# Kernel tuning notes

Measured on AMD Instinct MI355X. Metric: run time of the kernel, lower is better.

## Reference

```python
import jax, jax.numpy as jnp
import numpy as np

N, E, H, ED = 10000, 160000, 512, 16
EPS = 1e-5
EDGE_SCALE = 0.1

def _ln(x, g, b):
    mu = jnp.mean(x, axis=-1, keepdims=True)
    var = jnp.mean(jnp.square(x - mu), axis=-1, keepdims=True)
    return (x - mu) * jax.lax.rsqrt(var + EPS) * g + b

def setup_inputs() -> dict:
    key = jax.random.key(0)
    ks = jax.random.split(key, 16)
    def w(k, i, o):
        return jax.random.normal(k, (i, o), jnp.float32) * (1.0 / np.sqrt(i))
    return {
        "h": jax.random.normal(ks[0], (N, H), jnp.float32),
        "edge_attr": jax.random.normal(ks[1], (E, ED), jnp.float32),
        "msg_w1": w(ks[2], H + ED, H), "msg_b1": jnp.zeros((H,), jnp.float32),
        "msg_w2": w(ks[3], H, H),      "msg_b2": jnp.zeros((H,), jnp.float32),
        "upd_w1": w(ks[4], 2 * H, H),  "upd_b1": jnp.zeros((H,), jnp.float32),
        "upd_w2": w(ks[5], H, H),      "upd_b2": jnp.zeros((H,), jnp.float32),
        "norm_g": jnp.ones((H,), jnp.float32), "norm_b": jnp.zeros((H,), jnp.float32),
        "em_w1": w(ks[6], 2 * H + ED, ED), "em_b1": jnp.zeros((ED,), jnp.float32),
        "em_w2": w(ks[7], ED, ED),         "em_b2": jnp.zeros((ED,), jnp.float32),
        "eg_w": w(ks[8], 2 * H + ED, 1),   "eg_b": jnp.zeros((1,), jnp.float32),
        "en_g": jnp.ones((ED,), jnp.float32), "en_b": jnp.zeros((ED,), jnp.float32),
        "edge_index": jax.random.randint(ks[9], (2, E), 0, N, jnp.int32),
    }

def reference(h, edge_attr, msg_w1, msg_b1, msg_w2, msg_b2,
              upd_w1, upd_b1, upd_w2, upd_b2, norm_g, norm_b,
              em_w1, em_b1, em_w2, em_b2, eg_w, eg_b, en_g, en_b,
              edge_index):
    src, dst = edge_index[0], edge_index[1]
    hs = h[src]                      # (E, H)
    hd = h[dst]                      # (E, H)
    # edge update with gating + scaled residual (eval: keep mask == 1)
    z = jnp.concatenate([hs, hd, edge_attr], axis=-1)   # (E, 2H+ED)
    gate = jax.nn.sigmoid(z @ eg_w + eg_b)               # (E, 1)
    delta = jax.nn.gelu(z @ em_w1 + em_b1, approximate=False) @ em_w2 + em_b2
    e_new = _ln(edge_attr + EDGE_SCALE * gate * delta, en_g, en_b)
    # message computation + scatter-add aggregation
    zm = jnp.concatenate([hs, e_new], axis=-1)           # (E, H+ED)
    m = jax.nn.gelu(zm @ msg_w1 + msg_b1, approximate=False) @ msg_w2 + msg_b2
    agg = jax.ops.segment_sum(m, dst, num_segments=h.shape[0])  # (N, H)
    # node update + residual + LayerNorm
    zu = jnp.concatenate([h, agg], axis=-1)              # (N, 2H)
    h2 = jax.nn.gelu(zu @ upd_w1 + upd_b1, approximate=False) @ upd_w2 + upd_b2
    h_out = _ln(h + h2, norm_g, norm_b)
    return (h_out, e_new)
```

## Files before the change

kernel.cpp:

```cpp
#include <hip/hip_runtime.h>

#define N_NODES 10000
#define N_EDGES 160000
#define HD 512
#define EDD 16

typedef unsigned short u16;
typedef __attribute__((ext_vector_type(8))) short bf16x8;
typedef __attribute__((ext_vector_type(4))) float f32x4;
typedef unsigned int u32;

__device__ __forceinline__ float bf2f(u16 u){
  unsigned int x = ((unsigned int)u) << 16;
  return __builtin_bit_cast(float, x);
}
__device__ __forceinline__ u16 f2bf(float f){
  unsigned int x = __builtin_bit_cast(unsigned int, f);
  unsigned int r = (x + 0x7fffu + ((x >> 16) & 1u)) >> 16;
  return (u16)r;
}
__device__ __forceinline__ float ldx(const void* p, long long i, int f32){
  return f32 ? ((const float*)p)[i] : bf2f(((const u16*)p)[i]);
}
__device__ __forceinline__ void stx(void* p, long long i, int f32, float v){
  if (f32) ((float*)p)[i] = v; else ((u16*)p)[i] = f2bf(v);
}
__device__ __forceinline__ float gelu_f(float x){
  float c = x * x;
  float a = x * (1.5957691216f + 0.0713548162f * c);
  float e = __expf(-a);
  return x * __builtin_amdgcn_rcpf(1.0f + e);
}
__device__ __forceinline__ f32x4 mfma16(bf16x8 a, bf16x8 b, f32x4 c){
  return __builtin_amdgcn_mfma_f32_16x16x32_bf16(a, b, c, 0, 0, 0);
}
__device__ __forceinline__ int swz8(int row, int slot){
  return (slot ^ ((row >> 1) & 3)) * 8;
}
__device__ __forceinline__ bf16x8 ld8(const void* p, long long i, int f32){
  if (!f32) return *(const bf16x8*)((const u16*)p + i);
  const float* q = (const float*)p + i;
  float4 a = *(const float4*)q, b = *(const float4*)(q + 4);
  u16 t[8] = { f2bf(a.x), f2bf(a.y), f2bf(a.z), f2bf(a.w),
               f2bf(b.x), f2bf(b.y), f2bf(b.z), f2bf(b.w) };
  return *(const bf16x8*)t;
}
__device__ __forceinline__ void stage8(const void* src, long long idx, int f32, u16* dst){
  bf16x8 v = ld8(src, idx, f32);
  *(bf16x8*)dst = v;
}

__device__ __forceinline__ int probe_rand(const void* p, int l){
  const u16* q = (const u16*)p;
  float mx = 0.f;
  #pragma unroll
  for (int i = 0; i < 4; ++i) mx = fmaxf(mx, fabsf(bf2f(q[l * 4 + i])));
  #pragma unroll
  for (int m = 1; m < 64; m <<= 1) mx = fmaxf(mx, __shfl_xor(mx, m, 64));
  return (mx > 1e3f) ? 1 : 0;
}
__global__ __launch_bounds__(64) void kprobe(
    const void* h, const void* ea, const void* mw1, const void* mw2,
    const void* uw1, const void* uw2, const void* ew1, const void* ew2,
    const void* egw, const void* ng, const void* eng, int* F)
{
  const int l = threadIdx.x;
  int f0 = probe_rand(h, l),   f1 = probe_rand(ea, l),  f2 = probe_rand(mw1, l);
  int f3 = probe_rand(mw2, l), f4 = probe_rand(uw1, l), f5 = probe_rand(uw2, l);
  int f6 = probe_rand(ew1, l), f7 = probe_rand(ew2, l), f8 = probe_rand(egw, l);
  if (l == 0){
    F[0] = f0; F[1] = f1; F[2] = f2; F[3] = f3; F[4] = f4; F[5] = f5;
    F[6] = f6; F[7] = f7; F[8] = f8;
    F[9]  = (((const u16*)ng)[0]  == 0) ? 1 : 0;
    F[10] = (((const u16*)eng)[0] == 0) ? 1 : 0;
    F[11] = f0;
  }
}

__global__ void kfill(u16* __restrict__ out, long long n, float val){
  long long i = (long long)blockIdx.x * 256 + threadIdx.x;
  if (i < n) out[i] = f2bf(val);
}

__global__ __launch_bounds__(256) void kprep(
    const void* __restrict__ h, const void* __restrict__ mw1,
    const void* __restrict__ ew1, const void* __restrict__ egw,
    const void* __restrict__ mb2, const void* __restrict__ uw1,
    const int* __restrict__ F,
    u16* __restrict__ hB, u16* __restrict__ W1T, u16* __restrict__ WceT,
    float* __restrict__ bfused)
{
  __shared__ float tl[64][65];
  const int b = blockIdx.x, tid = threadIdx.x;
  if (b < 2500){
    const long long i = ((long long)b * 256 + tid) * 8;
    if (i < (long long)N_NODES * HD)
      *(bf16x8*)(hB + i) = ld8(h, i, F[0]);
  } else if (b < 2572){
    const int b2 = b - 2500;
    const int kt0 = (b2 >> 3) * 64, nt0 = (b2 & 7) * 64;
    const int ty = tid >> 6, tx = tid & 63;
    const int fw = F[2];
    #pragma unroll
    for (int q = 0; q < 16; ++q){
      const int r = ty * 16 + q;
      const int sr = kt0 + r;
      tl[r][tx] = (sr < 528) ? ldx(mw1, (long long)sr * 512 + nt0 + tx, fw) : 0.f;
    }
    __syncthreads();
    #pragma unroll
    for (int q = 0; q < 16; ++q){
      const int r = ty * 16 + q;
      const int k = kt0 + tx;
      if (k < 544) W1T[(size_t)(nt0 + r) * 544 + k] = f2bf(tl[tx][r]);
    }
  } else if (b < 2668){
    const int i = (b - 2572) * 256 + tid;
    const int c = i >> 9, k = i & 511;
    float v = 0.f;
    if (c < 16)       v = ldx(ew1, (long long)k * 16 + c, F[6]);
    else if (c < 32)  v = ldx(ew1, (long long)(512 + k) * 16 + (c - 16), F[6]);
    else if (c == 32) v = ldx(egw, k, F[8]);
    else if (c == 33) v = ldx(egw, 512 + k, F[8]);
    WceT[i] = f2bf(v);
  } else {
    float* ls   = &tl[0][0];
    float* part = &tl[0][0] + 1024;
    const int f3 = F[3], f4 = F[4];
    for (int j = tid; j < 512; j += 256) ls[j] = ldx(mb2, j, f3);
    __syncthreads();
    const int nn = tid & 31, jg = tid >> 5;
    const int n = (b - 2668) * 32 + nn;
    float a = 0.f;
    for (int jj = 0; jj < 64; ++jj){
      const int j = jg * 64 + jj;
      a += ls[j] * ldx(uw1, (long long)(512 + j) * 512 + n, f4);
    }
    part[jg * 33 + nn] = a;
    __syncthreads();
    if (jg == 0){
      float s = a;
      #pragma unroll
      for (int g = 1; g < 8; ++g) s += part[g * 33 + nn];
      bfused[n] = s;
    }
  }
}

__global__ __launch_bounds__(256) void kprep2(
    const void* __restrict__ uw1, const void* __restrict__ uw2,
    const int* __restrict__ F, u16* __restrict__ WU1T, u16* __restrict__ WU2T)
{
  __shared__ float tl[64][65];
  const int b = blockIdx.x, tid = threadIdx.x;
  const int ty = tid >> 6, tx = tid & 63;
  if (b < 128){
    const int kt0 = (b >> 3) * 64, nt0 = (b & 7) * 64;
    const int fw = F[4];
    #pragma unroll
    for (int q = 0; q < 16; ++q){
      const int r = ty * 16 + q;
      tl[r][tx] = ldx(uw1, (long long)(kt0 + r) * 512 + nt0 + tx, fw);
    }
    __syncthreads();
    #pragma unroll
    for (int q = 0; q < 16; ++q){
      const int r = ty * 16 + q;
      WU1T[(size_t)(nt0 + r) * 1024 + kt0 + tx] = f2bf(tl[tx][r]);
    }
  } else {
    const int b2 = b - 128;
    const int kt0 = (b2 >> 3) * 64, nt0 = (b2 & 7) * 64;
    const int fw = F[5];
    #pragma unroll
    for (int q = 0; q < 16; ++q){
      const int r = ty * 16 + q;
      tl[r][tx] = ldx(uw2, (long long)(kt0 + r) * 512 + nt0 + tx, fw);
    }
    __syncthreads();
    #pragma unroll
    for (int q = 0; q < 16; ++q){
      const int r = ty * 16 + q;
      WU2T[(size_t)(nt0 + r) * 512 + kt0 + tx] = f2bf(tl[tx][r]);
    }
  }
}

__global__ void kdeg(const int* __restrict__ dst, int* __restrict__ deg){
  int e = blockIdx.x * 256 + threadIdx.x;
  if (e < N_EDGES) atomicAdd(&deg[dst[e]], 1);
}

__global__ __launch_bounds__(256) void kscan(const int* __restrict__ deg,
                                             int* __restrict__ start){
  __shared__ int ls[256];
  const int t = threadIdx.x;
  const int base = t * 40;
  int s = 0;
  for (int i = 0; i < 40; ++i){ int idx = base + i; if (idx < N_NODES) s += deg[idx]; }
  ls[t] = s; __syncthreads();
  for (int off = 1; off < 256; off <<= 1){
    int v = (t >= off) ? ls[t - off] : 0;
    __syncthreads();
    ls[t] += v;
    __syncthreads();
  }
  int run = (t == 0) ? 0 : ls[t - 1];
  for (int i = 0; i < 40; ++i){
    int idx = base + i;
    if (idx < N_NODES){ start[idx] = run; run += deg[idx]; }
  }
}

__global__ void kscatter(const int* __restrict__ srcI, const int* __restrict__ dstI,
                         const int* __restrict__ start, int* __restrict__ cursor,
                         int* __restrict__ sSrc, int* __restrict__ sDst,
                         int* __restrict__ sIdx){
  int e = blockIdx.x * 256 + threadIdx.x;
  if (e < N_EDGES){
    int d = dstI[e];
    int p = start[d] + atomicAdd(&cursor[d], 1);
    sSrc[p] = srcI[e]; sDst[p] = d; sIdx[p] = e;
  }
}

__global__ __launch_bounds__(256, 4) void kprePE(
    const u16* __restrict__ hB, const u16* __restrict__ W1T,
    const void* __restrict__ msg_b1, const u16* __restrict__ WceT,
    const int* __restrict__ F, u16* __restrict__ P, u16* __restrict__ PE)
{
  __shared__ u16 As[128 * 32];
  __shared__ u16 Bs[64 * 32];
  const int tid = threadIdx.x;
  const int row0 = blockIdx.y * 128;
  const int w = tid >> 6, l = tid & 63;
  const int lm = l & 15, lk = l >> 4;
  if (blockIdx.x < 8){
    const int fw = F[2];
    const int n0 = blockIdx.x * 64;
    f32x4 acc[2][4];
    f32x4 z4 = {0.f, 0.f, 0.f, 0.f};
    #pragma unroll
    for (int i = 0; i < 2; ++i)
      #pragma unroll
      for (int j = 0; j < 4; ++j) acc[i][j] = z4;
    const int nB = tid >> 2, kqB = tid & 3;
    for (int kt = 0; kt < 16; ++kt){
      const int kk = kt * 32;
      #pragma unroll
      for (int i = 0; i < 2; ++i){
        int t = tid + i * 256;
        int m = t >> 2, kq = t & 3;
        int gr = row0 + m; if (gr > N_NODES - 1) gr = N_NODES - 1;
        *(uint4*)&As[m * 32 + swz8(m, kq)] = *(const uint4*)(hB + (size_t)gr * HD + kk + kq * 8);
      }
      *(uint4*)&Bs[nB * 32 + swz8(nB, kqB)] =
          *(const uint4*)(W1T + (size_t)(n0 + nB) * 544 + kk + kqB * 8);
      __syncthreads();
      bf16x8 af[2], bfv[4];
      #pragma unroll
      for (int i = 0; i < 2; ++i){
        const int R = w * 32 + i * 16 + lm;
        af[i] = *(const bf16x8*)&As[R * 32 + swz8(R, lk)];
      }
      #pragma unroll
      for (int j = 0; j < 4; ++j){
        const int R = j * 16 + lm;
        bfv[j] = *(const bf16x8*)&Bs[R * 32 + swz8(R, lk)];
      }
      #pragma unroll
      for (int i = 0; i < 2; ++i)
        #pragma unroll
        for (int j = 0; j < 4; ++j)
          acc[i][j] = mfma16(af[i], bfv[j], acc[i][j]);
      __syncthreads();
    }
    #pragma unroll
    for (int j = 0; j < 4; ++j){
      const int col = n0 + j * 16 + lm;
      const float bias = ldx(msg_b1, col, fw);
      #pragma unroll
      for (int i = 0; i < 2; ++i){
        const int rb = row0 + w * 32 + i * 16 + lk * 4;
        #pragma unroll
        for (int r = 0; r < 4; ++r){
          int gr = rb + r;
          if (gr < N_NODES)
            P[(size_t)gr * HD + col] = f2bf(acc[i][j][r] + bias);
        }
      }
    }
  } else {
    f32x4 acc[2][3];
    f32x4 z4 = {0.f, 0.f, 0.f, 0.f};
    #pragma unroll
    for (int i = 0; i < 2; ++i)
      #pragma unroll
      for (int j = 0; j < 3; ++j) acc[i][j] = z4;
    for (int kt = 0; kt < 16; ++kt){
      const int kk = kt * 32;
      #pragma unroll
      for (int i = 0; i < 2; ++i){
        int t = tid + i * 256;
        int m = t >> 2, kq = t & 3;
        int gr = row0 + m; if (gr > N_NODES - 1) gr = N_NODES - 1;
        *(uint4*)&As[m * 32 + swz8(m, kq)] = *(const uint4*)(hB + (size_t)gr * HD + kk + kq * 8);
      }
      if (tid < 192){
        int c = tid >> 2, kq = tid & 3;
        *(uint4*)&Bs[c * 32 + swz8(c, kq)] =
            *(const uint4*)(WceT + (size_t)c * 512 + kk + kq * 8);
      }
      __syncthreads();
      bf16x8 af[2], bfv[3];
      #pragma unroll
      for (int i = 0; i < 2; ++i){
        const int R = w * 32 + i * 16 + lm;
        af[i] = *(const bf16x8*)&As[R * 32 + swz8(R, lk)];
      }
      #pragma unroll
      for (int j = 0; j < 3; ++j){
        const int R = j * 16 + lm;
        bfv[j] = *(const bf16x8*)&Bs[R * 32 + swz8(R, lk)];
      }
      #pragma unroll
      for (int i = 0; i < 2; ++i)
        #pragma unroll
        for (int j = 0; j < 3; ++j)
          acc[i][j] = mfma16(af[i], bfv[j], acc[i][j]);
      __syncthreads();
    }
    #pragma unroll
    for (int j = 0; j < 3; ++j){
      const int col = j * 16 + lm;
      #pragma unroll
      for (int i = 0; i < 2; ++i){
        const int rb = row0 + w * 32 + i * 16 + lk * 4;
        #pragma unroll
        for (int r = 0; r < 4; ++r){
          int gr = rb + r;
          if (gr < N_NODES)
            PE[(size_t)gr * 48 + col] = f2bf(acc[i][j][r]);
        }
      }
    }
  }
}

__global__ __launch_bounds__(256) void kedge2(
    const void* __restrict__ ea, const u16* __restrict__ PE,
    const void* __restrict__ em_w1, const void* __restrict__ em_w2,
    const void* __restrict__ em_b1, const void* __restrict__ em_b2,
    const void* __restrict__ eg_w, const void* __restrict__ eg_b,
    const void* __restrict__ en_g, const void* __restrict__ en_b,
    const int* __restrict__ F,
    const int* __restrict__ srcI, const int* __restrict__ dstI,
    void* __restrict__ dout)
{
  __shared__ float wt[16][17];
  __shared__ float w2s[256];
  __shared__ float egt[16], b1e[16], b2s[16], gns[16], bns[16];
  __shared__ float egb_s;
  const int tid = threadIdx.x;
  const int fea = F[1], fem1 = F[6], fem2 = F[7], feg = F[8];
  const int fen = F[10], fo = F[11];
  { int k = tid >> 4, j = tid & 15;
    wt[k][j] = ldx(em_w1, (long long)(1024 + k) * 16 + j, fem1); }
  w2s[tid] = ldx(em_w2, tid, fem2);
  if (tid < 16){
    egt[tid] = ldx(eg_w, 1024 + tid, feg);
    b1e[tid] = ldx(em_b1, tid, fem1);
    b2s[tid] = ldx(em_b2, tid, fem2);
    gns[tid] = ldx(en_g, tid, fen);
    bns[tid] = ldx(en_b, tid, fen);
  }
  if (tid == 0) egb_s = ldx(eg_b, 0, feg);
  __syncthreads();

  const int e = blockIdx.x * 256 + tid;
  const int s = srcI[e], d = dstI[e];
  float earr[16];
  if (fea){
    const float4* q = (const float4*)((const float*)ea + (size_t)e * 16);
    float4 v0 = q[0], v1 = q[1], v2 = q[2], v3 = q[3];
    earr[0]=v0.x; earr[1]=v0.y; earr[2]=v0.z; earr[3]=v0.w;
    earr[4]=v1.x; earr[5]=v1.y; earr[6]=v1.z; earr[7]=v1.w;
    earr[8]=v2.x; earr[9]=v2.y; earr[10]=v2.z; earr[11]=v2.w;
    earr[12]=v3.x; earr[13]=v3.y; earr[14]=v3.z; earr[15]=v3.w;
  } else {
    const u16* q = (const u16*)ea + (size_t)e * 16;
    bf16x8 a = *(const bf16x8*)q, b = *(const bf16x8*)(q + 8);
    #pragma unroll
    for (int j = 0; j < 8; ++j){ earr[j] = bf2f((u16)a[j]); earr[8 + j] = bf2f((u16)b[j]); }
  }
  const u16* prs = PE + (size_t)s * 48;
  const u16* prd = PE + (size_t)d * 48;
  bf16x8 ps0 = *(const bf16x8*)prs,        ps1 = *(const bf16x8*)(prs + 8);
  bf16x8 pd0 = *(const bf16x8*)(prd + 16), pd1 = *(const bf16x8*)(prd + 24);
  const float gs = bf2f(prs[32]), gd = bf2f(prd[33]);
  float t[16];
  #pragma unroll
  for (int j = 0; j < 8; ++j){
    t[j]     = bf2f((u16)ps0[j]) + bf2f((u16)pd0[j]) + b1e[j];
    t[8 + j] = bf2f((u16)ps1[j]) + bf2f((u16)pd1[j]) + b1e[8 + j];
  }
  float gl = gs + gd + egb_s;
  #pragma unroll
  for (int k = 0; k < 16; ++k){
    const float ek = earr[k];
    gl += ek * egt[k];
    #pragma unroll
    for (int j = 0; j < 16; ++j) t[j] += ek * wt[k][j];
  }
  const float gate = __builtin_amdgcn_rcpf(1.0f + __expf(-gl));
  float gj[16];
  #pragma unroll
  for (int j = 0; j < 16; ++j) gj[j] = gelu_f(t[j]);
  float rv[16]; float s1 = 0.f, s2 = 0.f;
  #pragma unroll
  for (int j = 0; j < 16; ++j){
    float dlt = b2s[j];
    #pragma unroll
    for (int k = 0; k < 16; ++k) dlt += gj[k] * w2s[k * 16 + j];
    rv[j] = earr[j] + 0.1f * gate * dlt;
    s1 += rv[j]; s2 += rv[j] * rv[j];
  }
  const float mu  = s1 * (1.f / 16.f);
  const float var = s2 * (1.f / 16.f) - mu * mu;
  const float inv = rsqrtf(var + 1e-5f);
  if (fo){
    float* ob = (float*)dout + (size_t)N_NODES * HD + (size_t)e * 16;
    #pragma unroll
    for (int j = 0; j < 16; ++j) ob[j] = (rv[j] - mu) * inv * gns[j] + bns[j];
  } else {
    u16 tmp[16];
    #pragma unroll
    for (int j = 0; j < 16; ++j) tmp[j] = f2bf((rv[j] - mu) * inv * gns[j] + bns[j]);
    u16* ob = (u16*)dout + (size_t)N_NODES * HD + (size_t)e * 16;
    *(uint4*)ob = *(uint4*)&tmp[0];
    *(uint4*)(ob + 8) = *(uint4*)&tmp[8];
  }
}

__global__ __launch_bounds__(256, 4) void kWf(
    const u16* __restrict__ WU1T, const void* __restrict__ mw2,
    const int* __restrict__ F, u16* __restrict__ WfT)
{
  __shared__ u16 As[128 * 32];
  __shared__ u16 Bs[64 * 32];
  const int tid = threadIdx.x;
  const int f3 = F[3];
  const int row0 = blockIdx.y * 128, n0 = blockIdx.x * 64;
  f32x4 acc[2][4];
  f32x4 z4 = {0.f, 0.f, 0.f, 0.f};
  #pragma unroll
  for (int i = 0; i < 2; ++i)
    #pragma unroll
    for (int j = 0; j < 4; ++j) acc[i][j] = z4;
  const int w = tid >> 6, l = tid & 63;
  const int lm = l & 15, lk = l >> 4;
  const int nB = tid >> 2, kqB = tid & 3;
  for (int kt = 0; kt < 16; ++kt){
    const int kk = kt * 32;
    #pragma unroll
    for (int i = 0; i < 2; ++i){
      int t = tid + i * 256;
      int m = t >> 2, kq = t & 3;
      *(uint4*)&As[m * 32 + swz8(m, kq)] =
          *(const uint4*)(WU1T + (size_t)(row0 + m) * 1024 + 512 + kk + kq * 8);
    }
    stage8(mw2, (long long)(n0 + nB) * 512 + kk + kqB * 8, f3,
           &Bs[nB * 32 + swz8(nB, kqB)]);
    __syncthreads();
    bf16x8 af[2], bfv[4];
    #pragma unroll
    for (int i = 0; i < 2; ++i){
      const int R = w * 32 + i * 16 + lm;
      af[i] = *(const bf16x8*)&As[R * 32 + swz8(R, lk)];
    }
    #pragma unroll
    for (int j = 0; j < 4; ++j){
      const int R = j * 16 + lm;
      bfv[j] = *(const bf16x8*)&Bs[R * 32 + swz8(R, lk)];
    }
    #pragma unroll
    for (int i = 0; i < 2; ++i)
      #pragma unroll
      for (int j = 0; j < 4; ++j)
        acc[i][j] = mfma16(af[i], bfv[j], acc[i][j]);
    __syncthreads();
  }
  #pragma unroll
  for (int j = 0; j < 4; ++j){
    const int col = n0 + j * 16 + lm;
    #pragma unroll
    for (int i = 0; i < 2; ++i){
      const int rb = row0 + w * 32 + i * 16 + lk * 4;
      #pragma unroll
      for (int r = 0; r < 4; ++r)
        WfT[(size_t)(rb + r) * 512 + col] = f2bf(acc[i][j][r]);
    }
  }
}

__global__ __launch_bounds__(256, 4) void kmsg4(
    const u16* __restrict__ P, const void* __restrict__ dout,
    const u16* __restrict__ W1T, const int* __restrict__ F,
    const int* __restrict__ sSrc, const int* __restrict__ sDst,
    const int* __restrict__ sIdx,
    float* __restrict__ agg)
{
  __shared__ __align__(16) float SMEM[4352];
  u16*   As = (u16*)SMEM;
  u16*   Bs = (u16*)SMEM + 4096;
  float* Sf = SMEM;
  __shared__ int src_s[128];
  __shared__ int dst_s[128];
  const int tid = threadIdx.x;
  const int fo = F[11];
  const void* e_base = fo ? (const void*)((const float*)dout + (size_t)N_NODES * HD)
                          : (const void*)((const u16*)dout + (size_t)N_NODES * HD);
  const int row0 = blockIdx.x * 128, n0 = blockIdx.y * 128;
  if (tid < 128){
    src_s[tid] = sSrc[row0 + tid];
    dst_s[tid] = sDst[row0 + tid];
  }
  #pragma unroll
  for (int i = 0; i < 2; ++i){
    int t = tid + i * 256;
    int m = t >> 2, kq = t & 3;
    if (kq < 2){
      const long long ie = sIdx[row0 + m];
      stage8(e_base, ie * EDD + kq * 8, fo, &As[m * 32 + swz8(m, kq)]);
      *(uint4*)&Bs[m * 32 + swz8(m, kq)] =
          *(const uint4*)(W1T + (size_t)(n0 + m) * 544 + 512 + kq * 8);
    } else {
      uint4 z = {0,0,0,0};
      *(uint4*)&As[m * 32 + swz8(m, kq)] = z;
      *(uint4*)&Bs[m * 32 + swz8(m, kq)] = z;
    }
  }
  __syncthreads();
  const int w = tid >> 6, l = tid & 63;
  const int wr = w >> 1, wc = w & 1, lm = l & 15, lk = l >> 4;
  f32x4 acc[4][4];
  bf16x8 af[4], bfv[4];
  #pragma unroll
  for (int i = 0; i < 4; ++i){
    const int R = wr * 64 + i * 16 + lm;
    af[i] = *(const bf16x8*)&As[R * 32 + swz8(R, lk)];
  }
  #pragma unroll
  for (int j = 0; j < 4; ++j){
    const int R = wc * 64 + j * 16 + lm;
    bfv[j] = *(const bf16x8*)&Bs[R * 32 + swz8(R, lk)];
  }
  f32x4 z4 = {0.f, 0.f, 0.f, 0.f};
  #pragma unroll
  for (int i = 0; i < 4; ++i)
    #pragma unroll
    for (int j = 0; j < 4; ++j)
      acc[i][j] = mfma16(af[i], bfv[j], z4);
  u32 poff[4][4];
  #pragma unroll
  for (int i = 0; i < 4; ++i)
    #pragma unroll
    for (int r = 0; r < 4; ++r)
      poff[i][r] = (u32)src_s[wr * 64 + i * 16 + lk * 4 + r] * HD;
  float pv[4][16];
  {
    const int col0 = n0 + wc * 64 + lm;
    #pragma unroll
    for (int q = 0; q < 16; ++q)
      pv[0][q] = bf2f(P[poff[q >> 2][q & 3] + col0]);
  }
  const int cj = tid & 31, chunk = tid >> 5;
  const int rbase = chunk * 16;
  u32 aoff[16]; unsigned maskb = 0;
  {
    int dprev = dst_s[rbase];
    aoff[0] = (u32)dprev * HD;
    #pragma unroll
    for (int rr = 1; rr < 16; ++rr){
      const int dn = dst_s[rbase + rr];
      if (dn == dprev) maskb |= (1u << rr);
      aoff[rr] = (u32)dn * HD;
      dprev = dn;
    }
  }
  __syncthreads();
  const int sfb = wc * 16 + lm;
  #pragma unroll
  for (int j = 0; j < 4; ++j){
    if (j < 3){
      const int coln = n0 + wc * 64 + (j + 1) * 16 + lm;
      #pragma unroll
      for (int q = 0; q < 16; ++q)
        pv[j + 1][q] = bf2f(P[poff[q >> 2][q & 3] + coln]);
    }
    #pragma unroll
    for (int i = 0; i < 4; ++i)
      #pragma unroll
      for (int r = 0; r < 4; ++r){
        const int row = wr * 64 + i * 16 + lk * 4 + r;
        Sf[row * 34 + sfb] = gelu_f(acc[i][j][r] + pv[j][i * 4 + r]);
      }
    __syncthreads();
    const int acol = n0 + (cj >> 4) * 64 + j * 16 + (cj & 15);
    float run = Sf[rbase * 34 + cj];
    #pragma unroll
    for (int rr = 1; rr < 16; ++rr){
      const float v = Sf[(rbase + rr) * 34 + cj];
      if (maskb & (1u << rr)) run += v;
      else { atomicAdd(&agg[(size_t)aoff[rr - 1] + acol], run); run = v; }
    }
    atomicAdd(&agg[(size_t)aoff[15] + acol], run);
    __syncthreads();
  }
}

__global__ __launch_bounds__(256, 4) void kupd1f(
    const u16* __restrict__ hB, const float* __restrict__ S,
    const u16* __restrict__ WU1T, const u16* __restrict__ WfT,
    const void* __restrict__ upd_b1, const float* __restrict__ bfused,
    const int* __restrict__ deg, const int* __restrict__ F,
    u16* __restrict__ U)
{
  __shared__ u16 As[128 * 32];
  __shared__ u16 Bs[64 * 32];
  const int tid = threadIdx.x;
  const int fw = F[4];
  const int row0 = blockIdx.y * 128, n0 = blockIdx.x * 64;
  f32x4 acc[2][4];
  f32x4 z4 = {0.f, 0.f, 0.f, 0.f};
  #pragma unroll
  for (int i = 0; i < 2; ++i)
    #pragma unroll
    for (int j = 0; j < 4; ++j) acc[i][j] = z4;
  const int w = tid >> 6, l = tid & 63;
  const int lm = l & 15, lk = l >> 4;
  const int nB = tid >> 2, kqB = tid & 3;
  const int am = tid >> 1, ah = tid & 1;
  const int agr = row0 + am;
  for (int kt = 0; kt < 32; ++kt){
    const int kk = kt * 32;
    if (kk < 512){
      #pragma unroll
      for (int i = 0; i < 2; ++i){
        int t = tid + i * 256;
        int m = t >> 2, kq = t & 3;
        int gr = row0 + m; if (gr > N_NODES - 1) gr = N_NODES - 1;
        *(uint4*)&As[m * 32 + swz8(m, kq)] = *(const uint4*)(hB + (size_t)gr * HD + kk + kq * 8);
      }
      *(uint4*)&Bs[nB * 32 + swz8(nB, kqB)] =
          *(const uint4*)(WU1T + (size_t)(n0 + nB) * 1024 + kk + kqB * 8);
    } else {
      const int ks = kk - 512;
      u16 tmp[16];
      if (agr < N_NODES){
        const float4* sp = (const float4*)(S + (size_t)agr * HD + ks + ah * 16);
        #pragma unroll
        for (int q = 0; q < 4; ++q){
          float4 v = sp[q];
          tmp[q*4+0] = f2bf(v.x); tmp[q*4+1] = f2bf(v.y);
          tmp[q*4+2] = f2bf(v.z); tmp[q*4+3] = f2bf(v.w);
        }
      } else {
        #pragma unroll
        for (int q = 0; q < 16; ++q) tmp[q] = 0;
      }
      *(uint4*)&As[am * 32 + swz8(am, ah * 2)]     = *(uint4*)&tmp[0];
      *(uint4*)&As[am * 32 + swz8(am, ah * 2 + 1)] = *(uint4*)&tmp[8];
      *(uint4*)&Bs[nB * 32 + swz8(nB, kqB)] =
          *(const uint4*)(WfT + (size_t)(n0 + nB) * 512 + ks + kqB * 8);
    }
    __syncthreads();
    bf16x8 af[2], bfv[4];
    #pragma unroll
    for (int i = 0; i < 2; ++i){
      const int R = w * 32 + i * 16 + lm;
      af[i] = *(const bf16x8*)&As[R * 32 + swz8(R, lk)];
    }
    #pragma unroll
    for (int j = 0; j < 4; ++j){
      const int R = j * 16 + lm;
      bfv[j] = *(const bf16x8*)&Bs[R * 32 + swz8(R, lk)];
    }
    #pragma unroll
    for (int i = 0; i < 2; ++i)
      #pragma unroll
      for (int j = 0; j < 4; ++j)
        acc[i][j] = mfma16(af[i], bfv[j], acc[i][j]);
    __syncthreads();
  }
  #pragma unroll
  for (int j = 0; j < 4; ++j){
    const int col = n0 + j * 16 + lm;
    const float bias = ldx(upd_b1, col, fw);
    const float bfv2 = bfused[col];
    #pragma unroll
    for (int i = 0; i < 2; ++i){
      const int rb = row0 + w * 32 + i * 16 + lk * 4;
      #pragma unroll
      for (int r = 0; r < 4; ++r){
        int gr = rb + r;
        if (gr < N_NODES)
          U[(size_t)gr * HD + col] =
              f2bf(gelu_f(acc[i][j][r] + bias + (float)deg[gr] * bfv2));
      }
    }
  }
}

__global__ __launch_bounds__(256, 4) void kupd2(
    const u16* __restrict__ U, const u16* __restrict__ WU2T,
    const void* __restrict__ upd_b2, const int* __restrict__ F,
    u16* __restrict__ h2b)
{
  __shared__ u16 As[128 * 32];
  __shared__ u16 Bs[64 * 32];
  const int tid = threadIdx.x;
  const int fw = F[5];
  const int row0 = blockIdx.y * 128, n0 = blockIdx.x * 64;
  f32x4 acc[2][4];
  f32x4 z4 = {0.f, 0.f, 0.f, 0.f};
  #pragma unroll
  for (int i = 0; i < 2; ++i)
    #pragma unroll
    for (int j = 0; j < 4; ++j) acc[i][j] = z4;
  const int w = tid >> 6, l = tid & 63;
  const int lm = l & 15, lk = l >> 4;
  const int nB = tid >> 2, kqB = tid & 3;
  for (int kt = 0; kt < 16; ++kt){
    const int kk = kt * 32;
    #pragma unroll
    for (int i = 0; i < 2; ++i){
      int t = tid + i * 256;
      int m = t >> 2, kq = t & 3;
      int gr = row0 + m; if (gr > N_NODES - 1) gr = N_NODES - 1;
      *(uint4*)&As[m * 32 + swz8(m, kq)] = *(const uint4*)(U + (size_t)gr * HD + kk + kq * 8);
    }
    *(uint4*)&Bs[nB * 32 + swz8(nB, kqB)] =
        *(const uint4*)(WU2T + (size_t)(n0 + nB) * 512 + kk + kqB * 8);
    __syncthreads();
    bf16x8 af[2], bfv[4];
    #pragma unroll
    for (int i = 0; i < 2; ++i){
      const int R = w * 32 + i * 16 + lm;
      af[i] = *(const bf16x8*)&As[R * 32 + swz8(R, lk)];
    }
    #pragma unroll
    for (int j = 0; j < 4; ++j){
      const int R = j * 16 + lm;
      bfv[j] = *(const bf16x8*)&Bs[R * 32 + swz8(R, lk)];
    }
    #pragma unroll
    for (int i = 0; i < 2; ++i)
      #pragma unroll
      for (int j = 0; j < 4; ++j)
        acc[i][j] = mfma16(af[i], bfv[j], acc[i][j]);
    __syncthreads();
  }
  #pragma unroll
  for (int j = 0; j < 4; ++j){
    const int col = n0 + j * 16 + lm;
    const float bias = ldx(upd_b2, col, fw);
    #pragma unroll
    for (int i = 0; i < 2; ++i){
      const int rb = row0 + w * 32 + i * 16 + lk * 4;
      #pragma unroll
      for (int r = 0; r < 4; ++r){
        int gr = rb + r;
        if (gr < N_NODES)
          h2b[(size_t)gr * HD + col] = f2bf(acc[i][j][r] + bias);
      }
    }
  }
}

__global__ __launch_bounds__(256) void kln(
    const void* __restrict__ h, const u16* __restrict__ h2b,
    const void* __restrict__ gg, const void* __restrict__ bbv,
    const int* __restrict__ F, void* __restrict__ dout)
{
  const int fh = F[0], fng = F[9], fo = F[11];
  const int w = threadIdx.x >> 6, l = threadIdx.x & 63;
  const int row = blockIdx.x * 4 + w;
  float x[8];
  #pragma unroll
  for (int j = 0; j < 8; ++j){
    const long long idx = (long long)row * HD + l * 8 + j;
    x[j] = ldx(h, idx, fh) + bf2f(h2b[idx]);
  }
  float s1 = 0.f, s2 = 0.f;
  #pragma unroll
  for (int j = 0; j < 8; ++j){ s1 += x[j]; s2 += x[j] * x[j]; }
  #pragma unroll
  for (int m = 1; m < 64; m <<= 1){ s1 += __shfl_xor(s1, m, 64); s2 += __shfl_xor(s2, m, 64); }
  const float mu  = s1 * (1.f / 512.f);
  const float var = s2 * (1.f / 512.f) - mu * mu;
  const float inv = rsqrtf(var + 1e-5f);
  #pragma unroll
  for (int j = 0; j < 8; ++j){
    const float gf = ldx(gg,  l * 8 + j, fng);
    const float bf = ldx(bbv, l * 8 + j, fng);
    stx(dout, (long long)row * HD + l * 8 + j, fo, (x[j] - mu) * inv * gf + bf);
  }
}

#define OFF_S     0u
#define OFF_DEG   20480000u
#define OFF_CUR   20520000u
#define OFF_F     20560000u
#define OFF_START 20560064u
#define OFF_AGGM  20600064u
#define OFF_W1T   30840064u
#define OFF_W2T   31397120u
#define OFF_WU1T  31921408u
#define OFF_WU2T  32969984u
#define OFF_WET   33494272u
#define OFF_SSRC  33528064u
#define OFF_SDST  34168064u
#define OFF_SIDX  34808064u
#define WS_NEEDED 35448064u

extern "C" void kernel_launch(void* const* d_in, const int* in_sizes, int n_in,
                              void* d_out, int out_size, void* d_ws, size_t ws_size,
                              hipStream_t stream)
{
  const void* h      = d_in[0];
  const void* ea     = d_in[1];
  const void* msg_w1 = d_in[2];
  const void* msg_b1 = d_in[3];
  const void* msg_w2 = d_in[4];
  const void* msg_b2 = d_in[5];
  const void* upd_w1 = d_in[6];
  const void* upd_b1 = d_in[7];
  const void* upd_w2 = d_in[8];
  const void* upd_b2 = d_in[9];
  const void* norm_g = d_in[10];
  const void* norm_b = d_in[11];
  const void* em_w1  = d_in[12];
  const void* em_b1  = d_in[13];
  const void* em_w2  = d_in[14];
  const void* em_b2  = d_in[15];
  const void* eg_w   = d_in[16];
  const void* eg_b   = d_in[17];
  const void* en_g   = d_in[18];
  const void* en_b   = d_in[19];
  const int* eidx    = (const int*)d_in[20];
  const int* srcI = eidx;
  const int* dstI = eidx + N_EDGES;

  float sent = 0.f;
  if (ws_size < (size_t)WS_NEEDED)            sent = 1000.f;
  else if (n_in != 21)                        sent = 2000.f;
  else if (in_sizes[0]  != N_NODES * HD)      sent = 3000.f;
  else if (in_sizes[20] != 2 * N_EDGES)       sent = 4000.f;
  else if (out_size != N_NODES*HD + N_EDGES*EDD) sent = 5000.f;
  if (sent != 0.f){
    kfill<<<(out_size + 255)/256, 256, 0, stream>>>((u16*)d_out, out_size, sent);
    return;
  }

  char* ws = (char*)d_ws;
  float* S      = (float*)(ws + OFF_S);
  u16*   h2b    = (u16*)(ws + OFF_S);
  int*   deg    = (int*)(ws + OFF_DEG);
  int*   cur    = (int*)(ws + OFF_CUR);
  int*   F      = (int*)(ws + OFF_F);
  int*   start  = (int*)(ws + OFF_START);
  u16*   P      = (u16*)(ws + OFF_AGGM);
  u16*   U      = (u16*)(ws + OFF_AGGM);
  u16*   W1T    = (u16*)(ws + OFF_W1T);
  u16*   WfT    = (u16*)(ws + OFF_W2T);
  u16*   PE     = (u16*)(ws + OFF_WU1T);
  u16*   WU1T   = (u16*)(ws + OFF_WU1T);
  u16*   WceT   = (u16*)(ws + OFF_WU2T);
  u16*   WU2T   = (u16*)(ws + OFF_WU2T);
  float* bfused = (float*)(ws + OFF_WET);
  int*   sSrc   = (int*)(ws + OFF_SSRC);
  int*   sDst   = (int*)(ws + OFF_SDST);
  int*   sIdx   = (int*)(ws + OFF_SIDX);

  u16* hB = (u16*)d_out;

  hipMemsetAsync(S, 0, (size_t)OFF_F, stream);

  kprobe<<<1, 64, 0, stream>>>(h, ea, msg_w1, msg_w2, upd_w1, upd_w2,
                               em_w1, em_w2, eg_w, norm_g, en_g, F);

  kprep<<<2684, 256, 0, stream>>>(h, msg_w1, em_w1, eg_w, msg_b2, upd_w1, F,
                                  hB, W1T, WceT, bfused);

  kprePE<<<dim3(9, 79), 256, 0, stream>>>(hB, W1T, msg_b1, WceT, F, P, PE);

  kdeg<<<(N_EDGES + 255)/256, 256, 0, stream>>>(dstI, deg);
  kscan<<<1, 256, 0, stream>>>(deg, start);
  kscatter<<<(N_EDGES + 255)/256, 256, 0, stream>>>(srcI, dstI, start, cur,
                                                    sSrc, sDst, sIdx);

  kedge2<<<625, 256, 0, stream>>>(ea, PE, em_w1, em_w2, em_b1, em_b2, eg_w, eg_b,
                                  en_g, en_b, F, srcI, dstI, d_out);

  kprep2<<<192, 256, 0, stream>>>(upd_w1, upd_w2, F, WU1T, WU2T);
  kWf<<<dim3(8, 4), 256, 0, stream>>>(WU1T, msg_w2, F, WfT);

  kmsg4<<<dim3(1250, 4), 256, 0, stream>>>(P, d_out, W1T, F,
                                           sSrc, sDst, sIdx, S);
  kupd1f<<<dim3(8, 79), 256, 0, stream>>>(hB, S, WU1T, WfT, upd_b1, bfused,
                                          deg, F, U);
  kupd2<<<dim3(8, 79), 256, 0, stream>>>(U, WU2T, upd_b2, F, h2b);
  kln<<<2500, 256, 0, stream>>>(h, h2b, norm_g, norm_b, F, d_out);
}
```

Before: 407.2 us.

## Fold degree count, scan and Wf GEMM into existing prep kernels

Merges the degree-count atomics into extra blocks of kprep, the exclusive scan into an extra block column of kprePE, and the Wf weight GEMM into extra blocks of kprep2, reading upd_w1 directly with a strided transposing load. This removes three kernel launches and the gaps between them. In exchange, the Wf blocks do uncoalesced scalar loads instead of reusing the transposed WU1T. The scan runs in a grid of 79 rows where all but one block exit immediately.

```diff
diff --git a/kernel.cpp b/kernel.cpp
--- a/kernel.cpp
+++ b/kernel.cpp
@@ -86,9 +86,9 @@
     const void* __restrict__ h, const void* __restrict__ mw1,
     const void* __restrict__ ew1, const void* __restrict__ egw,
     const void* __restrict__ mb2, const void* __restrict__ uw1,
-    const int* __restrict__ F,
+    const int* __restrict__ dstI, const int* __restrict__ F,
     u16* __restrict__ hB, u16* __restrict__ W1T, u16* __restrict__ WceT,
-    float* __restrict__ bfused)
+    float* __restrict__ bfused, int* __restrict__ deg)
 {
   __shared__ float tl[64][65];
   const int b = blockIdx.x, tid = threadIdx.x;
@@ -123,7 +123,7 @@
     else if (c == 32) v = ldx(egw, k, F[8]);
     else if (c == 33) v = ldx(egw, 512 + k, F[8]);
     WceT[i] = f2bf(v);
-  } else {
+  } else if (b < 2684){
     float* ls   = &tl[0][0];
     float* part = &tl[0][0] + 1024;
     const int f3 = F[3], f4 = F[4];
@@ -144,12 +144,16 @@
       for (int g = 1; g < 8; ++g) s += part[g * 33 + nn];
       bfused[n] = s;
     }
+  } else {
+    const int e = (b - 2684) * 256 + tid;
+    if (e < N_EDGES) atomicAdd(&deg[dstI[e]], 1);
   }
 }
 
 __global__ __launch_bounds__(256) void kprep2(
     const void* __restrict__ uw1, const void* __restrict__ uw2,
-    const int* __restrict__ F, u16* __restrict__ WU1T, u16* __restrict__ WU2T)
+    const void* __restrict__ mw2, const int* __restrict__ F,
+    u16* __restrict__ WU1T, u16* __restrict__ WU2T, u16* __restrict__ WfT)
 {
   __shared__ float tl[64][65];
   const int b = blockIdx.x, tid = threadIdx.x;
@@ -168,7 +172,7 @@
       const int r = ty * 16 + q;
       WU1T[(size_t)(nt0 + r) * 1024 + kt0 + tx] = f2bf(tl[tx][r]);
     }
-  } else {
+  } else if (b < 192){
     const int b2 = b - 128;
     const int kt0 = (b2 >> 3) * 64, nt0 = (b2 & 7) * 64;
     const int fw = F[5];
@@ -183,32 +187,60 @@
       const int r = ty * 16 + q;
       WU2T[(size_t)(nt0 + r) * 512 + kt0 + tx] = f2bf(tl[tx][r]);
     }
-  }
-}
-
-__global__ void kdeg(const int* __restrict__ dst, int* __restrict__ deg){
-  int e = blockIdx.x * 256 + threadIdx.x;
-  if (e < N_EDGES) atomicAdd(&deg[dst[e]], 1);
-}
-
-__global__ __launch_bounds__(256) void kscan(const int* __restrict__ deg,
-                                             int* __restrict__ start){
-  __shared__ int ls[256];
-  const int t = threadIdx.x;
-  const int base = t * 40;
-  int s = 0;
-  for (int i = 0; i < 40; ++i){ int idx = base + i; if (idx < N_NODES) s += deg[idx]; }
-  ls[t] = s; __syncthreads();
-  for (int off = 1; off < 256; off <<= 1){
-    int v = (t >= off) ? ls[t - off] : 0;
-    __syncthreads();
-    ls[t] += v;
-    __syncthreads();
-  }
-  int run = (t == 0) ? 0 : ls[t - 1];
-  for (int i = 0; i < 40; ++i){
-    int idx = base + i;
-    if (idx < N_NODES){ start[idx] = run; run += deg[idx]; }
+  } else {
+    u16* As2 = (u16*)&tl[0][0];
+    u16* Bs2 = (u16*)&tl[0][0] + 4096;
+    const int b2 = b - 192;
+    const int row0 = (b2 >> 3) * 128, n0 = (b2 & 7) * 64;
+    const int f3 = F[3], f4 = F[4];
+    f32x4 acc[2][4];
+    f32x4 z4 = {0.f, 0.f, 0.f, 0.f};
+    #pragma unroll
+    for (int i = 0; i < 2; ++i)
+      #pragma unroll
+      for (int j = 0; j < 4; ++j) acc[i][j] = z4;
+    const int w = tid >> 6, l = tid & 63;
+    const int lm = l & 15, lk = l >> 4;
+    const int nB = tid >> 2, kqB = tid & 3;
+    for (int kt = 0; kt < 16; ++kt){
+      const int kk = kt * 32;
+      for (int idx = tid; idx < 4096; idx += 256){
+        const int kc = idx >> 7, m = idx & 127;
+        As2[m * 32 + swz8(m, kc >> 3) + (kc & 7)] =
+            f2bf(ldx(uw1, (long long)(512 + kk + kc) * 512 + row0 + m, f4));
+      }
+      stage8(mw2, (long long)(n0 + nB) * 512 + kk + kqB * 8, f3,
+             &Bs2[nB * 32 + swz8(nB, kqB)]);
+      __syncthreads();
+      bf16x8 af[2], bfv[4];
+      #pragma unroll
+      for (int i = 0; i < 2; ++i){
+        const int R = w * 32 + i * 16 + lm;
+        af[i] = *(const bf16x8*)&As2[R * 32 + swz8(R, lk)];
+      }
+      #pragma unroll
+      for (int j = 0; j < 4; ++j){
+        const int R = j * 16 + lm;
+        bfv[j] = *(const bf16x8*)&Bs2[R * 32 + swz8(R, lk)];
+      }
+      #pragma unroll
+      for (int i = 0; i < 2; ++i)
+        #pragma unroll
+        for (int j = 0; j < 4; ++j)
+          acc[i][j] = mfma16(af[i], bfv[j], acc[i][j]);
+      __syncthreads();
+    }
+    #pragma unroll
+    for (int j = 0; j < 4; ++j){
+      const int col = n0 + j * 16 + lm;
+      #pragma unroll
+      for (int i = 0; i < 2; ++i){
+        const int rb = row0 + w * 32 + i * 16 + lk * 4;
+        #pragma unroll
+        for (int r = 0; r < 4; ++r)
+          WfT[(size_t)(rb + r) * 512 + col] = f2bf(acc[i][j][r]);
+      }
+    }
   }
 }
 
@@ -227,7 +259,8 @@
 __global__ __launch_bounds__(256, 4) void kprePE(
     const u16* __restrict__ hB, const u16* __restrict__ W1T,
     const void* __restrict__ msg_b1, const u16* __restrict__ WceT,
-    const int* __restrict__ F, u16* __restrict__ P, u16* __restrict__ PE)
+    const int* __restrict__ deg, const int* __restrict__ F,
+    u16* __restrict__ P, u16* __restrict__ PE, int* __restrict__ start)
 {
   __shared__ u16 As[128 * 32];
   __shared__ u16 Bs[64 * 32];
@@ -290,7 +323,7 @@
         }
       }
     }
-  } else {
+  } else if (blockIdx.x == 8){
     f32x4 acc[2][3];
     f32x4 z4 = {0.f, 0.f, 0.f, 0.f};
     #pragma unroll
@@ -343,6 +376,25 @@
             PE[(size_t)gr * 48 + col] = f2bf(acc[i][j][r]);
         }
       }
+    }
+  } else {
+    if (blockIdx.y != 0) return;
+    int* ls = (int*)As;
+    const int t = tid;
+    const int base = t * 40;
+    int s = 0;
+    for (int i = 0; i < 40; ++i){ int idx = base + i; if (idx < N_NODES) s += deg[idx]; }
+    ls[t] = s; __syncthreads();
+    for (int off = 1; off < 256; off <<= 1){
+      int v = (t >= off) ? ls[t - off] : 0;
+      __syncthreads();
+      ls[t] += v;
+      __syncthreads();
+    }
+    int run = (t == 0) ? 0 : ls[t - 1];
+    for (int i = 0; i < 40; ++i){
+      int idx = base + i;
+      if (idx < N_NODES){ start[idx] = run; run += deg[idx]; }
     }
   }
 }
@@ -439,67 +491,6 @@
     u16* ob = (u16*)dout + (size_t)N_NODES * HD + (size_t)e * 16;
     *(uint4*)ob = *(uint4*)&tmp[0];
     *(uint4*)(ob + 8) = *(uint4*)&tmp[8];
-  }
-}
-
-__global__ __launch_bounds__(256, 4) void kWf(
-    const u16* __restrict__ WU1T, const void* __restrict__ mw2,
-    const int* __restrict__ F, u16* __restrict__ WfT)
-{
-  __shared__ u16 As[128 * 32];
-  __shared__ u16 Bs[64 * 32];
-  const int tid = threadIdx.x;
-  const int f3 = F[3];
-  const int row0 = blockIdx.y * 128, n0 = blockIdx.x * 64;
-  f32x4 acc[2][4];
-  f32x4 z4 = {0.f, 0.f, 0.f, 0.f};
-  #pragma unroll
-  for (int i = 0; i < 2; ++i)
-    #pragma unroll
-    for (int j = 0; j < 4; ++j) acc[i][j] = z4;
-  const int w = tid >> 6, l = tid & 63;
-  const int lm = l & 15, lk = l >> 4;
-  const int nB = tid >> 2, kqB = tid & 3;
-  for (int kt = 0; kt < 16; ++kt){
-    const int kk = kt * 32;
-    #pragma unroll
-    for (int i = 0; i < 2; ++i){
-      int t = tid + i * 256;
-      int m = t >> 2, kq = t & 3;
-      *(uint4*)&As[m * 32 + swz8(m, kq)] =
-          *(const uint4*)(WU1T + (size_t)(row0 + m) * 1024 + 512 + kk + kq * 8);
-    }
-    stage8(mw2, (long long)(n0 + nB) * 512 + kk + kqB * 8, f3,
-           &Bs[nB * 32 + swz8(nB, kqB)]);
-    __syncthreads();
-    bf16x8 af[2], bfv[4];
-    #pragma unroll
-    for (int i = 0; i < 2; ++i){
-      const int R = w * 32 + i * 16 + lm;
-      af[i] = *(const bf16x8*)&As[R * 32 + swz8(R, lk)];
-    }
-    #pragma unroll
-    for (int j = 0; j < 4; ++j){
-      const int R = j * 16 + lm;
-      bfv[j] = *(const bf16x8*)&Bs[R * 32 + swz8(R, lk)];
-    }
-    #pragma unroll
-    for (int i = 0; i < 2; ++i)
-      #pragma unroll
-      for (int j = 0; j < 4; ++j)
-        acc[i][j] = mfma16(af[i], bfv[j], acc[i][j]);
-    __syncthreads();
-  }
-  #pragma unroll
-  for (int j = 0; j < 4; ++j){
-    const int col = n0 + j * 16 + lm;
-    #pragma unroll
-    for (int i = 0; i < 2; ++i){
-      const int rb = row0 + w * 32 + i * 16 + lk * 4;
-      #pragma unroll
-      for (int r = 0; r < 4; ++r)
-        WfT[(size_t)(rb + r) * 512 + col] = f2bf(acc[i][j][r]);
-    }
   }
 }
 
@@ -890,21 +881,19 @@
   kprobe<<<1, 64, 0, stream>>>(h, ea, msg_w1, msg_w2, upd_w1, upd_w2,
                                em_w1, em_w2, eg_w, norm_g, en_g, F);
 
-  kprep<<<2684, 256, 0, stream>>>(h, msg_w1, em_w1, eg_w, msg_b2, upd_w1, F,
-                                  hB, W1T, WceT, bfused);
-
-  kprePE<<<dim3(9, 79), 256, 0, stream>>>(hB, W1T, msg_b1, WceT, F, P, PE);
-
-  kdeg<<<(N_EDGES + 255)/256, 256, 0, stream>>>(dstI, deg);
-  kscan<<<1, 256, 0, stream>>>(deg, start);
+  kprep<<<3309, 256, 0, stream>>>(h, msg_w1, em_w1, eg_w, msg_b2, upd_w1,
+                                  dstI, F, hB, W1T, WceT, bfused, deg);
+
+  kprePE<<<dim3(10, 79), 256, 0, stream>>>(hB, W1T, msg_b1, WceT, deg, F,
+                                           P, PE, start);
+
   kscatter<<<(N_EDGES + 255)/256, 256, 0, stream>>>(srcI, dstI, start, cur,
                                                     sSrc, sDst, sIdx);
 
   kedge2<<<625, 256, 0, stream>>>(ea, PE, em_w1, em_w2, em_b1, em_b2, eg_w, eg_b,
                                   en_g, en_b, F, srcI, dstI, d_out);
 
-  kprep2<<<192, 256, 0, stream>>>(upd_w1, upd_w2, F, WU1T, WU2T);
-  kWf<<<dim3(8, 4), 256, 0, stream>>>(WU1T, msg_w2, F, WfT);
+  kprep2<<<224, 256, 0, stream>>>(upd_w1, upd_w2, msg_w2, F, WU1T, WU2T, WfT);
 
   kmsg4<<<dim3(1250, 4), 256, 0, stream>>>(P, d_out, W1T, F,
                                            sSrc, sDst, sIdx, S);
```

Result: slower. 456.9 us (+12.2%).
